# Optimization experiments

Measured on AMD Instinct MI355X. Metric: run time of the kernel, lower is better.

Reference implementation:

```python
import jax, jax.numpy as jnp
import numpy as np

B, N, R = 16, 512, 10
DE, DR, DOUT = 256, 64, 256

def setup_inputs() -> dict:
    key = jax.random.key(0)
    k1, k2, k3, k4 = jax.random.split(key, 4)
    node_features = jax.random.normal(k1, (B, N, DE), dtype=jnp.float32)
    relation_features = jax.random.normal(k2, (B, R, DR), dtype=jnp.float32)
    adj = jax.random.uniform(k3, (B, R, N, N), dtype=jnp.float32)
    in_dim = (DE + DR) * R
    bound = float(np.sqrt(6.0 / (in_dim + DOUT)))  # xavier_uniform
    W = jax.random.uniform(k4, (DOUT, in_dim), dtype=jnp.float32, minval=-bound, maxval=bound)
    bias = jnp.zeros((DOUT,), dtype=jnp.float32)
    return {"node_features": node_features, "relation_features": relation_features,
            "adj": adj, "W": W, "bias": bias}

def reference(node_features, relation_features, adj, W, bias):
    # adj: [B,R,N,N]; node_features: [B,N,De]; relation_features: [B,R,Dr]
    # Per relation r: bmm(adj[:,r], cat([node, rel_r broadcast], -1))
    # Node part: adj @ node_features for every relation at once.
    node_part = jnp.einsum('brnm,bmd->brnd', adj, node_features)      # [B,R,N,De]
    # Relation part: adj @ (rel_r repeated over rows) == rowsum(adj) * rel_r
    rel_part = adj.sum(axis=-1)[..., None] * relation_features[:, :, None, :]  # [B,R,N,Dr]
    supports = jnp.concatenate([node_part, rel_part], axis=-1)        # [B,R,N,De+Dr]
    supports = supports.transpose(0, 2, 1, 3).reshape(node_features.shape[0],
                                                      node_features.shape[1], -1)  # [B,N,R*(De+Dr)]
    return supports @ W.T + bias
```

## Files before the change

kernel.cpp:

```cpp
#include <hip/hip_runtime.h>
#include <stdint.h>

#define B_     16
#define N_     512
#define R_     10
#define DE_    256
#define DR_    64
#define DOUT_  256
#define INDIM_ 3200
#define BLK_   320
#define RN_    5120
#define SPLITS_ 5

typedef __bf16          v8bf  __attribute__((ext_vector_type(8)));
typedef unsigned short  v8us  __attribute__((ext_vector_type(8)));
typedef unsigned short  v4us  __attribute__((ext_vector_type(4)));
typedef float           f32x4 __attribute__((ext_vector_type(4)));

static __device__ __forceinline__ unsigned short f2b(float f) {
  union { float f; unsigned u; } c; c.f = f;
  unsigned r = c.u + 0x7FFFu + ((c.u >> 16) & 1u);
  return (unsigned short)(r >> 16);
}

static __device__ __forceinline__ v8bf us2bf(v8us u) {
  union { v8us u; v8bf b; } c; c.u = u; return c.b;
}

static __device__ __forceinline__ void gl_lds16(const void* g, void* l) {
  __builtin_amdgcn_global_load_lds(
      (const __attribute__((address_space(1))) void*)g,
      (__attribute__((address_space(3))) void*)l, 16, 0, 0);
}

__global__ void prep_all(const float* __restrict__ nf, const float* __restrict__ W,
                         const float* __restrict__ rel,
                         unsigned short* __restrict__ nodeB,
                         unsigned short* __restrict__ WnB,
                         float* __restrict__ Uf) {
  const int bb = blockIdx.x;
  const int tid = threadIdx.x;
  if (bb < 256) {
    const size_t base = (size_t)bb * 8192;
#pragma unroll
    for (int p = 0; p < 4; ++p) {
      size_t off = base + (size_t)p * 2048 + (size_t)tid * 8;
      float4 x = *(const float4*)(nf + off);
      float4 y = *(const float4*)(nf + off + 4);
      v8us u;
      u[0] = f2b(x.x); u[1] = f2b(x.y); u[2] = f2b(x.z); u[3] = f2b(x.w);
      u[4] = f2b(y.x); u[5] = f2b(y.y); u[6] = f2b(y.z); u[7] = f2b(y.w);
      *(v8us*)(nodeB + off) = u;
    }
  } else if (bb < 896) {
    int idx = (bb - 256) * 1024 + tid * 4;
    int r = idx >> 16;
    int o = (idx >> 8) & 255;
    int d = idx & 255;
    float4 x = *(const float4*)(W + (size_t)o * INDIM_ + r * BLK_ + d);
    v4us u;
    u[0] = f2b(x.x); u[1] = f2b(x.y); u[2] = f2b(x.z); u[3] = f2b(x.w);
    *(v4us*)(WnB + idx) = u;
  } else {
    int idx = (bb - 896) * 256 + tid;
    int o  = idx & 255;
    int br = idx >> 8;
    int r  = br % R_;
    const float* rp = rel + (size_t)br * DR_;
    const float* wp = W + (size_t)o * INDIM_ + r * BLK_ + DE_;
    float v = 0.f;
#pragma unroll 8
    for (int d = 0; d < DR_; ++d) v += rp[d] * wp[d];
    Uf[idx] = v;
  }
}

__global__ void stageA_gemm(const unsigned short* __restrict__ nodeB,
                            const unsigned short* __restrict__ WnB,
                            const float* __restrict__ Uf,
                            unsigned short* __restrict__ Gp) {
  __shared__ unsigned short S[128 * 128];
  unsigned short* Al = S;
  unsigned short* Bl = S + 128 * 64;
  const int br = blockIdx.x;
  const int b  = br / R_, r = br % R_;
  const int o0 = blockIdx.y * 128;
  const int m0 = blockIdx.z * 128;
  const int tid  = threadIdx.x;
  const int lane = tid & 63;
  const int wave = tid >> 6;
  const int wm = wave >> 1, wn = wave & 1;
  const int quad = lane >> 4, l16 = lane & 15;

  const unsigned short* Wb = WnB + (size_t)r * (DOUT_ * DE_);
  const unsigned short* Nb = nodeB + (size_t)b * (N_ * DE_);

  f32x4 acc[4][4];
#pragma unroll
  for (int i = 0; i < 4; ++i)
#pragma unroll
    for (int j = 0; j < 4; ++j) acc[i][j] = f32x4{0.f, 0.f, 0.f, 0.f};

  for (int dk = 0; dk < DE_; dk += 64) {
#pragma unroll
    for (int it = 0; it < 4; ++it) {
      int rowblk = it * 32 + wave * 8;
      int rl = rowblk + (lane >> 3);
      int kc = (lane & 7) ^ (rl & 7);
      gl_lds16(Wb + (size_t)(o0 + rl) * DE_ + dk + kc * 8, Al + rowblk * 64);
      gl_lds16(Nb + (size_t)(m0 + rl) * DE_ + dk + kc * 8, Bl + rowblk * 64);
    }
    __syncthreads();
#pragma unroll
    for (int ks = 0; ks < 2; ++ks) {
      const int kb = ks * 4;
      v8bf av[4], bv[4];
#pragma unroll
      for (int mi = 0; mi < 4; ++mi) {
        int m = wm * 64 + mi * 16 + l16;
        av[mi] = us2bf(*(const v8us*)(Al + m * 64 + (((kb + quad) ^ (m & 7)) * 8)));
      }
#pragma unroll
      for (int ni = 0; ni < 4; ++ni) {
        int c = wn * 64 + ni * 16 + l16;
        bv[ni] = us2bf(*(const v8us*)(Bl + c * 64 + (((kb + quad) ^ (c & 7)) * 8)));
      }
#pragma unroll
      for (int mi = 0; mi < 4; ++mi)
#pragma unroll
        for (int ni = 0; ni < 4; ++ni)
          acc[mi][ni] = __builtin_amdgcn_mfma_f32_16x16x32_bf16(av[mi], bv[ni], acc[mi][ni], 0, 0, 0);
    }
    __syncthreads();
  }

#pragma unroll
  for (int mi = 0; mi < 4; ++mi)
#pragma unroll
    for (int t = 0; t < 4; ++t) {
      int o_loc = wm * 64 + mi * 16 + quad * 4 + t;
      float u = Uf[(size_t)br * DOUT_ + o0 + o_loc];
#pragma unroll
      for (int ni = 0; ni < 4; ++ni) {
        int m_loc = wn * 64 + ni * 16 + l16;
        S[o_loc * 128 + m_loc] = f2b(acc[mi][ni][t] + u);
      }
    }
  __syncthreads();
#pragma unroll
  for (int p = 0; p < 8; ++p) {
    int idx16 = p * 2048 + tid * 8;
    int orow = idx16 >> 7;
    int moff = idx16 & 127;
    unsigned short* dst = Gp + ((size_t)(b * DOUT_ + o0 + orow)) * RN_ + r * N_ + m0 + moff;
    *(v8us*)dst = *(const v8us*)(S + idx16);
  }
}

__global__ __launch_bounds__(256, 4)
void stageB_gemm(const float* __restrict__ adj,
                 const unsigned short* __restrict__ Gp,
                 float* __restrict__ part) {
  __shared__ unsigned short Al[32 * 64];
  __shared__ unsigned short Bl[256 * 64];
  const int b  = blockIdx.x;
  const int n0 = blockIdx.y * 32;
  const int sp = blockIdx.z;
  const int tid  = threadIdx.x;
  const int lane = tid & 63;
  const int wave = tid >> 6;
  const int quad = lane >> 4, l16 = lane & 15;

  const float* Ab = adj + (size_t)b * (R_ * N_ * N_);
  const unsigned short* Gb = Gp + (size_t)b * (DOUT_ * RN_);

  f32x4 acc[2][4];
#pragma unroll
  for (int i = 0; i < 2; ++i)
#pragma unroll
    for (int j = 0; j < 4; ++j) acc[i][j] = f32x4{0.f, 0.f, 0.f, 0.f};

  const int arow = tid >> 3;
  const int ac8  = tid & 7;
  const float* arp = Ab + (size_t)(n0 + arow) * N_ + ac8 * 8;

  float4 p0, p1;
  {
    const float* g = arp + (size_t)(sp * 2) * (N_ * N_);
    p0 = *(const float4*)(g);
    p1 = *(const float4*)(g + 4);
  }

  for (int it = 0; it < 16; ++it) {
    const int r  = sp * 2 + (it >> 3);
    const int k0 = r * N_ + (it & 7) * 64;
#pragma unroll
    for (int s = 0; s < 8; ++s) {
      int rowblk = s * 32 + wave * 8;
      int rl = rowblk + (lane >> 3);
      int kc = (lane & 7) ^ (rl & 7);
      gl_lds16(Gb + (size_t)rl * RN_ + k0 + kc * 8, Bl + rowblk * 64);
    }
    {
      v8us u;
      u[0] = f2b(p0.x); u[1] = f2b(p0.y); u[2] = f2b(p0.z); u[3] = f2b(p0.w);
      u[4] = f2b(p1.x); u[5] = f2b(p1.y); u[6] = f2b(p1.z); u[7] = f2b(p1.w);
      int cs = ac8 ^ (arow & 7);
      *(v8us*)(Al + arow * 64 + cs * 8) = u;
    }
    if (it < 15) {
      const int rn = sp * 2 + ((it + 1) >> 3);
      const float* g = arp + (size_t)rn * (N_ * N_) + ((it + 1) & 7) * 64;
      p0 = *(const float4*)(g);
      p1 = *(const float4*)(g + 4);
    }
    __syncthreads();
#pragma unroll
    for (int ks = 0; ks < 2; ++ks) {
      const int kb = ks * 4;
      v8bf av[2], bv[4];
#pragma unroll
      for (int mi = 0; mi < 2; ++mi) {
        int m = mi * 16 + l16;
        av[mi] = us2bf(*(const v8us*)(Al + m * 64 + (((kb + quad) ^ (m & 7)) * 8)));
      }
#pragma unroll
      for (int ni = 0; ni < 4; ++ni) {
        int o = wave * 64 + ni * 16 + l16;
        bv[ni] = us2bf(*(const v8us*)(Bl + o * 64 + (((kb + quad) ^ (o & 7)) * 8)));
      }
#pragma unroll
      for (int mi = 0; mi < 2; ++mi)
#pragma unroll
        for (int ni = 0; ni < 4; ++ni)
          acc[mi][ni] = __builtin_amdgcn_mfma_f32_16x16x32_bf16(av[mi], bv[ni], acc[mi][ni], 0, 0, 0);
    }
    __syncthreads();
  }

  float* pb = part + (((size_t)sp * B_ + b) * N_) * DOUT_;
#pragma unroll
  for (int mi = 0; mi < 2; ++mi)
#pragma unroll
    for (int t = 0; t < 4; ++t) {
      int row = n0 + mi * 16 + quad * 4 + t;
#pragma unroll
      for (int ni = 0; ni < 4; ++ni) {
        int col = wave * 64 + ni * 16 + l16;
        pb[(size_t)row * DOUT_ + col] = acc[mi][ni][t];
      }
    }
}

__global__ void reduce_out(const float* __restrict__ part, const float* __restrict__ bias,
                           float* __restrict__ out) {
  const size_t idx = (size_t)blockIdx.x * 256 + threadIdx.x;
  const size_t stride = (size_t)B_ * N_ * DOUT_ / 4;
  f32x4 a = *(const f32x4*)(bias + (idx & 63) * 4);
#pragma unroll
  for (int s = 0; s < SPLITS_; ++s) {
    f32x4 p = *(const f32x4*)((const float*)part + (stride * s + idx) * 4);
    a += p;
  }
  *(f32x4*)(out + idx * 4) = a;
}

extern "C" void kernel_launch(void* const* d_in, const int* in_sizes, int n_in,
                              void* d_out, int out_size, void* d_ws, size_t ws_size,
                              hipStream_t stream) {
  const float* node = (const float*)d_in[0];
  const float* rel  = (const float*)d_in[1];
  const float* adj  = (const float*)d_in[2];
  const float* W    = (const float*)d_in[3];
  const float* bias = (const float*)d_in[4];
  float* out = (float*)d_out;

  char* ws = (char*)d_ws;
  unsigned short* nodeB = (unsigned short*)(ws);
  unsigned short* WnB   = (unsigned short*)(ws + ((size_t)5 << 20));
  float*          Uf    = (float*)         (ws + ((size_t)7 << 20));
  unsigned short* Gp    = (unsigned short*)(ws + ((size_t)8 << 20));
  float*          part  = (float*)         (ws + ((size_t)48 << 20));

  prep_all<<<dim3(1056), 256, 0, stream>>>(node, W, rel, nodeB, WnB, Uf);
  stageA_gemm<<<dim3(B_ * R_, DOUT_ / 128, N_ / 128), 256, 0, stream>>>(nodeB, WnB, Uf, Gp);
  stageB_gemm<<<dim3(B_, N_ / 32, SPLITS_), 256, 0, stream>>>(adj, Gp, part);
  reduce_out<<<dim3((B_ * N_ * DOUT_ / 4) / 256), 256, 0, stream>>>(part, bias, out);
}
```

Measured before the change: 313.7 us.

## Enlarge stage-B tile to 128x256 with double-buffered LDS and fewer K splits

The stage-B GEMM now gives each block 128 output rows instead of 32 and runs 512 threads in a 2x4 wave grid. It double-buffers the adjacency and Gp tiles in LDS so the next chunk's loads overlap the current chunk's MFMAs, and drops the K split count from 5 to 4 with 20 chunks per split. Each Gp tile is now reused across four times as many rows, which cuts redundant reads of Gp. In exchange the grid shrinks to 256 blocks with larger register and LDS use per block, which may leave CUs underused.

```diff
diff --git a/kernel.cpp b/kernel.cpp
--- a/kernel.cpp
+++ b/kernel.cpp
@@ -10,7 +10,8 @@
 #define INDIM_ 3200
 #define BLK_   320
 #define RN_    5120
-#define SPLITS_ 5
+#define SPLITS_ 4
+#define CPS_    20
 
 typedef __bf16          v8bf  __attribute__((ext_vector_type(8)));
 typedef unsigned short  v8us  __attribute__((ext_vector_type(8)));
@@ -157,97 +158,129 @@
   }
 }
 
-__global__ __launch_bounds__(256, 4)
+__global__ __launch_bounds__(512, 2)
 void stageB_gemm(const float* __restrict__ adj,
                  const unsigned short* __restrict__ Gp,
                  float* __restrict__ part) {
-  __shared__ unsigned short Al[32 * 64];
-  __shared__ unsigned short Bl[256 * 64];
+  __shared__ unsigned short SB[2 * 24576];
   const int b  = blockIdx.x;
-  const int n0 = blockIdx.y * 32;
+  const int n0 = blockIdx.y * 128;
   const int sp = blockIdx.z;
   const int tid  = threadIdx.x;
   const int lane = tid & 63;
   const int wave = tid >> 6;
+  const int wm = wave >> 2;
+  const int wn = wave & 3;
   const int quad = lane >> 4, l16 = lane & 15;
 
   const float* Ab = adj + (size_t)b * (R_ * N_ * N_);
   const unsigned short* Gb = Gp + (size_t)b * (DOUT_ * RN_);
 
-  f32x4 acc[2][4];
-#pragma unroll
-  for (int i = 0; i < 2; ++i)
+  f32x4 acc[4][4];
+#pragma unroll
+  for (int i = 0; i < 4; ++i)
 #pragma unroll
     for (int j = 0; j < 4; ++j) acc[i][j] = f32x4{0.f, 0.f, 0.f, 0.f};
 
-  const int arow = tid >> 3;
-  const int ac8  = tid & 7;
-  const float* arp = Ab + (size_t)(n0 + arow) * N_ + ac8 * 8;
-
-  float4 p0, p1;
+  const int ar0 = tid >> 3;
+  const int ac8 = tid & 7;
+  const int acs = ac8 ^ (ar0 & 7);
+  const int brl = wave * 8 + (lane >> 3);
+  const int bkc = lane & 7;
+
+  int c = sp * CPS_;
+
   {
-    const float* g = arp + (size_t)(sp * 2) * (N_ * N_);
-    p0 = *(const float4*)(g);
-    p1 = *(const float4*)(g + 4);
-  }
-
-  for (int it = 0; it < 16; ++it) {
-    const int r  = sp * 2 + (it >> 3);
-    const int k0 = r * N_ + (it & 7) * 64;
-#pragma unroll
-    for (int s = 0; s < 8; ++s) {
-      int rowblk = s * 32 + wave * 8;
-      int rl = rowblk + (lane >> 3);
-      int kc = (lane & 7) ^ (rl & 7);
-      gl_lds16(Gb + (size_t)rl * RN_ + k0 + kc * 8, Bl + rowblk * 64);
-    }
-    {
-      v8us u;
-      u[0] = f2b(p0.x); u[1] = f2b(p0.y); u[2] = f2b(p0.z); u[3] = f2b(p0.w);
-      u[4] = f2b(p1.x); u[5] = f2b(p1.y); u[6] = f2b(p1.z); u[7] = f2b(p1.w);
-      int cs = ac8 ^ (arow & 7);
-      *(v8us*)(Al + arow * 64 + cs * 8) = u;
-    }
-    if (it < 15) {
-      const int rn = sp * 2 + ((it + 1) >> 3);
-      const float* g = arp + (size_t)rn * (N_ * N_) + ((it + 1) & 7) * 64;
-      p0 = *(const float4*)(g);
-      p1 = *(const float4*)(g + 4);
-    }
-    __syncthreads();
+    const int r = c >> 3, m0 = (c & 7) << 6, k0 = c << 6;
+    unsigned short* Aln = SB;
+    unsigned short* Bln = SB + 128 * 64;
+#pragma unroll
+    for (int s = 0; s < 4; ++s) {
+      int rl = s * 64 + brl;
+      int kc = bkc ^ (rl & 7);
+      gl_lds16(Gb + (size_t)rl * RN_ + k0 + kc * 8, Bln + (s * 64 + wave * 8) * 64);
+    }
+    const float* Ap = Ab + ((size_t)r * N_ + n0) * N_ + m0;
+    float4 a0 = *(const float4*)(Ap + (size_t)ar0 * N_ + ac8 * 8);
+    float4 a1 = *(const float4*)(Ap + (size_t)ar0 * N_ + ac8 * 8 + 4);
+    float4 a2 = *(const float4*)(Ap + (size_t)(ar0 + 64) * N_ + ac8 * 8);
+    float4 a3 = *(const float4*)(Ap + (size_t)(ar0 + 64) * N_ + ac8 * 8 + 4);
+    v8us u0, u1;
+    u0[0] = f2b(a0.x); u0[1] = f2b(a0.y); u0[2] = f2b(a0.z); u0[3] = f2b(a0.w);
+    u0[4] = f2b(a1.x); u0[5] = f2b(a1.y); u0[6] = f2b(a1.z); u0[7] = f2b(a1.w);
+    u1[0] = f2b(a2.x); u1[1] = f2b(a2.y); u1[2] = f2b(a2.z); u1[3] = f2b(a2.w);
+    u1[4] = f2b(a3.x); u1[5] = f2b(a3.y); u1[6] = f2b(a3.z); u1[7] = f2b(a3.w);
+    *(v8us*)(Aln + ar0 * 64 + acs * 8) = u0;
+    *(v8us*)(Aln + (ar0 + 64) * 64 + acs * 8) = u1;
+  }
+  __syncthreads();
+
+  for (int t = 0; t < CPS_; ++t) {
+    unsigned short* Sc = SB + (t & 1) * 24576;
+    unsigned short* Sn = SB + ((t & 1) ^ 1) * 24576;
+    float4 a0, a1, a2, a3;
+    const bool pf = (t + 1 < CPS_);
+    if (pf) {
+      const int c1 = c + 1;
+      const int r = c1 >> 3, m0 = (c1 & 7) << 6, k0 = c1 << 6;
+      unsigned short* Bln = Sn + 128 * 64;
+#pragma unroll
+      for (int s = 0; s < 4; ++s) {
+        int rl = s * 64 + brl;
+        int kc = bkc ^ (rl & 7);
+        gl_lds16(Gb + (size_t)rl * RN_ + k0 + kc * 8, Bln + (s * 64 + wave * 8) * 64);
+      }
+      const float* Ap = Ab + ((size_t)r * N_ + n0) * N_ + m0;
+      a0 = *(const float4*)(Ap + (size_t)ar0 * N_ + ac8 * 8);
+      a1 = *(const float4*)(Ap + (size_t)ar0 * N_ + ac8 * 8 + 4);
+      a2 = *(const float4*)(Ap + (size_t)(ar0 + 64) * N_ + ac8 * 8);
+      a3 = *(const float4*)(Ap + (size_t)(ar0 + 64) * N_ + ac8 * 8 + 4);
+    }
+    const unsigned short* Alc = Sc;
+    const unsigned short* Blc = Sc + 128 * 64;
 #pragma unroll
     for (int ks = 0; ks < 2; ++ks) {
       const int kb = ks * 4;
-      v8bf av[2], bv[4];
-#pragma unroll
-      for (int mi = 0; mi < 2; ++mi) {
-        int m = mi * 16 + l16;
-        av[mi] = us2bf(*(const v8us*)(Al + m * 64 + (((kb + quad) ^ (m & 7)) * 8)));
+      v8bf av[4], bv[4];
+#pragma unroll
+      for (int mi = 0; mi < 4; ++mi) {
+        int m = wm * 64 + mi * 16 + l16;
+        av[mi] = us2bf(*(const v8us*)(Alc + m * 64 + (((kb + quad) ^ (m & 7)) * 8)));
       }
 #pragma unroll
       for (int ni = 0; ni < 4; ++ni) {
-        int o = wave * 64 + ni * 16 + l16;
-        bv[ni] = us2bf(*(const v8us*)(Bl + o * 64 + (((kb + quad) ^ (o & 7)) * 8)));
-      }
-#pragma unroll
-      for (int mi = 0; mi < 2; ++mi)
+        int o = wn * 64 + ni * 16 + l16;
+        bv[ni] = us2bf(*(const v8us*)(Blc + o * 64 + (((kb + quad) ^ (o & 7)) * 8)));
+      }
+#pragma unroll
+      for (int mi = 0; mi < 4; ++mi)
 #pragma unroll
         for (int ni = 0; ni < 4; ++ni)
           acc[mi][ni] = __builtin_amdgcn_mfma_f32_16x16x32_bf16(av[mi], bv[ni], acc[mi][ni], 0, 0, 0);
     }
+    if (pf) {
+      v8us u0, u1;
+      u0[0] = f2b(a0.x); u0[1] = f2b(a0.y); u0[2] = f2b(a0.z); u0[3] = f2b(a0.w);
+      u0[4] = f2b(a1.x); u0[5] = f2b(a1.y); u0[6] = f2b(a1.z); u0[7] = f2b(a1.w);
+      u1[0] = f2b(a2.x); u1[1] = f2b(a2.y); u1[2] = f2b(a2.z); u1[3] = f2b(a2.w);
+      u1[4] = f2b(a3.x); u1[5] = f2b(a3.y); u1[6] = f2b(a3.z); u1[7] = f2b(a3.w);
+      *(v8us*)(Sn + ar0 * 64 + acs * 8) = u0;
+      *(v8us*)(Sn + (ar0 + 64) * 64 + acs * 8) = u1;
+    }
     __syncthreads();
+    ++c;
   }
 
   float* pb = part + (((size_t)sp * B_ + b) * N_) * DOUT_;
 #pragma unroll
-  for (int mi = 0; mi < 2; ++mi)
-#pragma unroll
-    for (int t = 0; t < 4; ++t) {
-      int row = n0 + mi * 16 + quad * 4 + t;
+  for (int mi = 0; mi < 4; ++mi)
+#pragma unroll
+    for (int t4 = 0; t4 < 4; ++t4) {
+      int row = n0 + wm * 64 + mi * 16 + quad * 4 + t4;
 #pragma unroll
       for (int ni = 0; ni < 4; ++ni) {
-        int col = wave * 64 + ni * 16 + l16;
-        pb[(size_t)row * DOUT_ + col] = acc[mi][ni][t];
+        int col = wn * 64 + ni * 16 + l16;
+        pb[(size_t)row * DOUT_ + col] = acc[mi][ni][t4];
       }
     }
 }
@@ -284,6 +317,6 @@
 
   prep_all<<<dim3(1056), 256, 0, stream>>>(node, W, rel, nodeB, WnB, Uf);
   stageA_gemm<<<dim3(B_ * R_, DOUT_ / 128, N_ / 128), 256, 0, stream>>>(nodeB, WnB, Uf, Gp);
-  stageB_gemm<<<dim3(B_, N_ / 32, SPLITS_), 256, 0, stream>>>(adj, Gp, part);
+  stageB_gemm<<<dim3(B_, N_ / 128, SPLITS_), 512, 0, stream>>>(adj, Gp, part);
   reduce_out<<<dim3((B_ * N_ * DOUT_ / 4) / 256), 256, 0, stream>>>(part, bias, out);
 }
```

Result: faster. 291.1 us (-7.2%).
